# Performance work log

Measured on AMD Instinct MI355X. Metric: run time of the kernel, lower is better.

## Reference

```python
import jax, jax.numpy as jnp
import numpy as np
import math

HGT, WID = 24, 24          # shape2d
NUM_HEADS = 12
EMB = 768
HEAD_DIM = EMB // NUM_HEADS
N_GRID = HGT * WID         # 576 spatial tokens
N_TOK = N_GRID + 1         # +1 CLS token
BATCH = 32


def _rel_indices(h: int, w: int) -> np.ndarray:
    """[(h*w), (h*w)] indices into the (2h-1)*(2w-1) relative table."""
    y = np.arange(h)
    x = np.arange(w)
    y1, x1, y2, x2 = np.meshgrid(y, x, y, x, indexing='ij')
    idx = (y1 - y2 + h - 1) * (2 * w - 1) + (x1 - x2 + w - 1)
    return idx.reshape(h * w, h * w)


def setup_inputs() -> dict:
    key = jax.random.key(0)
    ks = jax.random.split(key, 6)
    s = 0.02
    return {
        "x": jax.random.normal(ks[0], (BATCH, N_TOK, EMB), dtype=jnp.float32),
        "Wq": jax.random.normal(ks[1], (EMB, EMB), dtype=jnp.float32) * s,
        "bq": jnp.zeros((EMB,), dtype=jnp.float32),
        "Wk": jax.random.normal(ks[2], (EMB, EMB), dtype=jnp.float32) * s,
        "bk": jnp.zeros((EMB,), dtype=jnp.float32),
        "Wv": jax.random.normal(ks[3], (EMB, EMB), dtype=jnp.float32) * s,
        "bv": jnp.zeros((EMB,), dtype=jnp.float32),
        "Wp": jax.random.normal(ks[4], (EMB, EMB), dtype=jnp.float32) * s,
        "bp": jnp.zeros((EMB,), dtype=jnp.float32),
        "rel_table": jax.random.normal(ks[5], ((2 * HGT - 1) * (2 * WID - 1), NUM_HEADS), dtype=jnp.float32) * s,
    }


def reference(x, Wq, bq, Wk, bk, Wv, bv, Wp, bp, rel_table):
    B, N, E = x.shape
    scale = 1.0 / math.sqrt(HEAD_DIM)

    def heads(t):  # [B,N,E] -> [B,H,N,hd]
        return t.reshape(B, N, NUM_HEADS, HEAD_DIM).transpose(0, 2, 1, 3)

    q = heads(x @ Wq.T + bq)
    k = heads(x @ Wk.T + bk)
    v = heads(x @ Wv.T + bv)

    scores = jnp.einsum('bhqd,bhkd->bhqk', q, k) * scale  # [B,H,N,N]

    # relative position bias on spatial tokens (skip CLS row/col)
    idx = jnp.asarray(_rel_indices(HGT, WID))              # [Ng,Ng]
    bias = rel_table[idx].transpose(2, 0, 1)               # [H,Ng,Ng]
    scores = scores.at[:, :, 1:, 1:].add(bias)

    attn = jax.nn.softmax(scores, axis=-1)
    out = jnp.einsum('bhqk,bhkd->bhqd', attn, v)           # [B,H,N,hd]
    out = out.transpose(0, 2, 1, 3).reshape(B, N, E)
    return out @ Wp.T + bp
```

## Files before the change

### kernel.cpp

```cpp
#include <hip/hip_runtime.h>
#include <stdint.h>

#define HGT   24
#define WID   24
#define NHEAD 12
#define EMB   768
#define HD    64
#define NGRID 576
#define NTOK  577
#define NPAD  640
#define BATCH 32
#define MROWS (BATCH * NTOK)
#define NKT   10
#define NQT   5
#define QKVC  (3 * EMB)

typedef __attribute__((ext_vector_type(8))) short bf16x8;
typedef __attribute__((ext_vector_type(4))) float f32x4;

__device__ __forceinline__ short f2bf(float f) {
    union { float f; unsigned u; } c; c.f = f;
    unsigned r = (c.u + 0x7FFFu + ((c.u >> 16) & 1u)) >> 16;
    return (short)(r & 0xFFFFu);
}
__device__ __forceinline__ float b2f(short s) {
    union { unsigned u; float f; } c; c.u = ((unsigned)(unsigned short)s) << 16;
    return c.f;
}

__device__ __forceinline__ void gload16(void* lds, const void* g) {
    __builtin_amdgcn_global_load_lds(
        (const __attribute__((address_space(1))) void*)g,
        (__attribute__((address_space(3))) void*)lds, 16, 0, 0);
}

__device__ __forceinline__ void wait_vm0_barrier() {
    asm volatile("s_waitcnt vmcnt(0)" ::: "memory");
    __builtin_amdgcn_s_barrier();
}

__device__ __forceinline__ int xcd_swizzle(int orig, int nwg) {
    int q = nwg >> 3, r = nwg & 7;
    int xcd = orig & 7, idx = orig >> 3;
    return (xcd < r) ? xcd * (q + 1) + idx : r * (q + 1) + (xcd - r) * q + idx;
}

__global__ void cast_f32_bf16(const float* __restrict__ src, short* __restrict__ dst, int n) {
    int i = (blockIdx.x * blockDim.x + threadIdx.x) * 4;
    int stride = gridDim.x * blockDim.x * 4;
    for (int j = i; j < n; j += stride) {
        float4 v = *(const float4*)(src + j);
        short4 o;
        o.x = f2bf(v.x); o.y = f2bf(v.y); o.z = f2bf(v.z); o.w = f2bf(v.w);
        *(short4*)(dst + j) = o;
    }
}

__global__ void bias_expand(const float* __restrict__ rel, short* __restrict__ be) {
    int q = blockIdx.x;
    int k = threadIdx.x;
    float v[NHEAD];
    if (k >= NTOK) {
#pragma unroll
        for (int h = 0; h < NHEAD; h++) v[h] = -1e30f;
    } else if (q == 0 || q >= NTOK || k == 0) {
#pragma unroll
        for (int h = 0; h < NHEAD; h++) v[h] = 0.f;
    } else {
        int i = q - 1, j = k - 1;
        int idx = ((i / WID) - (j / WID) + HGT - 1) * (2 * WID - 1)
                + ((i % WID) - (j % WID) + WID - 1);
        const float* rp = rel + (size_t)idx * NHEAD;
#pragma unroll
        for (int h = 0; h < NHEAD; h++) v[h] = rp[h];
    }
#pragma unroll
    for (int h = 0; h < NHEAD; h++)
        be[((size_t)h * NPAD + q) * NPAD + k] = f2bf(v[h]);
}

__global__ __launch_bounds__(256) void transpose_v(const short* __restrict__ qnat, short* __restrict__ vt) {
    __shared__ __align__(16) short T[64][72];
    int bi = blockIdx.x;
    int kt = bi % NKT;
    int h  = (bi / NKT) % NHEAD;
    int b  = bi / (NKT * NHEAD);
    int t  = threadIdx.x;

    int r  = t >> 2, cb = (t & 3) * 16;
    int key = kt * 64 + r; if (key >= NTOK) key = NTOK - 1;
    const short* src = qnat + (size_t)(b * NTOK + key) * QKVC + 2 * EMB + h * HD;
    *(int4*)&T[r][cb]     = *(const int4*)(src + cb);
    *(int4*)&T[r][cb + 8] = *(const int4*)(src + cb + 8);
    __syncthreads();

    int d = t >> 2, kb = (t & 3) * 16;
    short tmp[16];
#pragma unroll
    for (int s = 0; s < 16; s++) tmp[s] = T[kb + s][d];
    short* dst = vt + (((size_t)b * NHEAD + h) * HD + d) * NPAD + kt * 64 + kb;
    *(int4*)&dst[0] = *(int4*)&tmp[0];
    *(int4*)&dst[8] = *(int4*)&tmp[8];
}

template <int MODE>
__global__ __launch_bounds__(512) void gemm_bt(
    const short* __restrict__ A, const short* __restrict__ Bw,
    const float* __restrict__ b0, const float* __restrict__ b1, const float* __restrict__ b2,
    void* __restrict__ Outp, int M)
{
    constexpr int NC  = (MODE == 0) ? QKVC : EMB;
    constexpr int NBX = NC / 256;
    constexpr int K   = EMB;
    constexpr int NST = K / 32;

    __shared__ __align__(16) short Asl[4][256][32];
    __shared__ __align__(16) short Bsl[4][256][32];

    const int t    = threadIdx.x;
    const int lane = t & 63;
    const int w    = t >> 6;
    const int wm   = w >> 2;
    const int wn   = w & 3;
    const int lg   = lane >> 4;
    const int li   = lane & 15;

    const int nwg  = NBX * ((MROWS + 255) / 256);
    const int wgid = xcd_swizzle(blockIdx.x, nwg);
    const int tm   = (wgid / NBX) * 256;
    const int tn   = (wgid % NBX) * 256;

    const int drow = lane >> 2;
    const int lc   = (lane & 3) ^ ((lane >> 3) & 3);
    const int xsw  = (li >> 1) & 3;

    const short* agp[2];
    const short* bgp[2];
#pragma unroll
    for (int gi = 0; gi < 2; gi++) {
        int rm = tm + gi * 128 + w * 16 + drow; if (rm >= M) rm = M - 1;
        agp[gi] = A  + (size_t)rm * K + lc * 8;
        bgp[gi] = Bw + (size_t)(tn + gi * 128 + w * 16 + drow) * K + lc * 8;
    }

    f32x4 acc[8][4];
#pragma unroll
    for (int i = 0; i < 8; i++)
#pragma unroll
        for (int j = 0; j < 4; j++) acc[i][j] = (f32x4){0.f, 0.f, 0.f, 0.f};

#pragma unroll
    for (int ss = 0; ss < 3; ss++) {
        gload16(&Asl[ss][0 * 128 + w * 16][0], agp[0] + ss * 32);
        gload16(&Asl[ss][1 * 128 + w * 16][0], agp[1] + ss * 32);
        gload16(&Bsl[ss][0 * 128 + w * 16][0], bgp[0] + ss * 32);
        gload16(&Bsl[ss][1 * 128 + w * 16][0], bgp[1] + ss * 32);
    }

    for (int s = 0; s < NST; s++) {
        if (s < NST - 2)       asm volatile("s_waitcnt vmcnt(8)" ::: "memory");
        else if (s == NST - 2) asm volatile("s_waitcnt vmcnt(4)" ::: "memory");
        else                   asm volatile("s_waitcnt vmcnt(0)" ::: "memory");
        __builtin_amdgcn_s_barrier();

        const int cb = s & 3;
        bf16x8 af[8], bfv[4];
#pragma unroll
        for (int mi = 0; mi < 8; mi++)
            af[mi] = *(const bf16x8*)&Asl[cb][wm * 128 + mi * 16 + li][(lg ^ xsw) * 8];
#pragma unroll
        for (int nj = 0; nj < 4; nj++)
            bfv[nj] = *(const bf16x8*)&Bsl[cb][wn * 64 + nj * 16 + li][(lg ^ xsw) * 8];

        if (s + 3 < NST) {
            const int tb = (s + 3) & 3;
            const int ko = (s + 3) * 32;
            gload16(&Asl[tb][0 * 128 + w * 16][0], agp[0] + ko);
            gload16(&Asl[tb][1 * 128 + w * 16][0], agp[1] + ko);
            gload16(&Bsl[tb][0 * 128 + w * 16][0], bgp[0] + ko);
            gload16(&Bsl[tb][1 * 128 + w * 16][0], bgp[1] + ko);
        }

        __builtin_amdgcn_s_setprio(1);
#pragma unroll
        for (int mi = 0; mi < 8; mi++)
#pragma unroll
            for (int nj = 0; nj < 4; nj++)
                acc[mi][nj] = __builtin_amdgcn_mfma_f32_16x16x32_bf16(
                    bfv[nj], af[mi], acc[mi][nj], 0, 0, 0);
        __builtin_amdgcn_s_setprio(0);
    }

#pragma unroll
    for (int nj = 0; nj < 4; nj++) {
        const int ccb = tn + wn * 64 + nj * 16 + lg * 4;
        float4 bias4;
        if constexpr (MODE == 0) {
            int which = (ccb >= 2 * EMB) ? 2 : ((ccb >= EMB) ? 1 : 0);
            const float* bb = (which == 0) ? b0 : ((which == 1) ? b1 : b2);
            bias4 = *(const float4*)&bb[ccb - which * EMB];
        } else {
            bias4 = *(const float4*)&b0[ccb];
        }
#pragma unroll
        for (int mi = 0; mi < 8; mi++) {
            int m = tm + wm * 128 + mi * 16 + li;
            if (m >= M) continue;
            if constexpr (MODE == 0) {
                short4 o;
                o.x = f2bf(acc[mi][nj][0] + bias4.x);
                o.y = f2bf(acc[mi][nj][1] + bias4.y);
                o.z = f2bf(acc[mi][nj][2] + bias4.z);
                o.w = f2bf(acc[mi][nj][3] + bias4.w);
                *(short4*)&((short*)Outp)[(size_t)m * NC + ccb] = o;
            } else {
                float4 o;
                o.x = acc[mi][nj][0] + bias4.x;
                o.y = acc[mi][nj][1] + bias4.y;
                o.z = acc[mi][nj][2] + bias4.z;
                o.w = acc[mi][nj][3] + bias4.w;
                *(float4*)&((float*)Outp)[(size_t)m * NC + ccb] = o;
            }
        }
    }
}

__global__ __launch_bounds__(512) void attn_kernel(
    const short* __restrict__ qnat, const short* __restrict__ vt,
    const short* __restrict__ biasx, short* __restrict__ aout)
{
    __shared__ __align__(16) short Ksl[2][64][64];
    __shared__ __align__(16) short Vsl[2][64][64];
    __shared__ __align__(16) short Psl[8][16][72];

    const int wg = (blockIdx.x & 7) * (BATCH * NHEAD * NQT / 8) + (blockIdx.x >> 3);
    const int qt = wg % NQT;
    const int rest = wg / NQT;
    const int b  = rest & 31;
    const int h  = rest >> 5;

    const int t    = threadIdx.x;
    const int lane = t & 63;
    const int w    = t >> 6;
    const int lg   = lane >> 4;
    const int li   = lane & 15;
    const int xh   = li & 7;
    const int qbase = qt * 128;
    const int myq  = qbase + w * 16 + li;

    const short* qp  = qnat + (size_t)b * NTOK * QKVC + h * HD;
    const short* kp  = qp + EMB;
    const short* vtp = vt + ((size_t)b * NHEAD + h) * (size_t)HD * NPAD;
    const short* browq = biasx + ((size_t)h * NPAD + myq) * NPAD;

    bf16x8 qf[2];
    {
        int qrow = myq < NTOK ? myq : NTOK - 1;
        qf[0] = *(const bf16x8*)(qp + (size_t)qrow * QKVC + lg * 8);
        qf[1] = *(const bf16x8*)(qp + (size_t)qrow * QKVC + 32 + lg * 8);
    }

    float mrun = -1e30f, lrun = 0.f;
    f32x4 oacc[4];
#pragma unroll
    for (int d = 0; d < 4; d++) oacc[d] = (f32x4){0.f, 0.f, 0.f, 0.f};

    const int srow = w * 8 + (lane >> 3);
    const int cofs = ((lane & 7) ^ (lane >> 3)) * 8;

    {
        int key = srow; if (key >= NTOK) key = NTOK - 1;
        gload16(&Ksl[0][w * 8][0], kp + (size_t)key * QKVC + cofs);
        gload16(&Vsl[0][w * 8][0], vtp + (size_t)srow * NPAD + cofs);
    }
    wait_vm0_barrier();

    short (*Kc)[64] = Ksl[0], (*Kn)[64] = Ksl[1];
    short (*Vc)[64] = Vsl[0], (*Vn)[64] = Vsl[1];

    for (int kt = 0; kt < NKT; kt++) {
        if (kt + 1 < NKT) {
            int key = (kt + 1) * 64 + srow; if (key >= NTOK) key = NTOK - 1;
            gload16(&Kn[w * 8][0], kp + (size_t)key * QKVC + cofs);
            gload16(&Vn[w * 8][0], vtp + (size_t)srow * NPAD + (kt + 1) * 64 + cofs);
        }

        float pvv[4][4];
        __builtin_amdgcn_s_setprio(1);
#pragma unroll
        for (int j = 0; j < 4; j++) {
            short4 bs = *(const short4*)&browq[kt * 64 + j * 16 + lg * 4];
            bf16x8 ak0 = *(const bf16x8*)&Kc[j * 16 + li][(lg ^ xh) * 8];
            bf16x8 ak1 = *(const bf16x8*)&Kc[j * 16 + li][((4 + lg) ^ xh) * 8];
            f32x4 s = (f32x4){0.f, 0.f, 0.f, 0.f};
            s = __builtin_amdgcn_mfma_f32_16x16x32_bf16(ak0, qf[0], s, 0, 0, 0);
            s = __builtin_amdgcn_mfma_f32_16x16x32_bf16(ak1, qf[1], s, 0, 0, 0);
            pvv[j][0] = fmaf(s[0], 0.125f, b2f(bs.x));
            pvv[j][1] = fmaf(s[1], 0.125f, b2f(bs.y));
            pvv[j][2] = fmaf(s[2], 0.125f, b2f(bs.z));
            pvv[j][3] = fmaf(s[3], 0.125f, b2f(bs.w));
        }
        __builtin_amdgcn_s_setprio(0);

        float mt = pvv[0][0];
#pragma unroll
        for (int j = 0; j < 4; j++)
#pragma unroll
            for (int r = 0; r < 4; r++) mt = fmaxf(mt, pvv[j][r]);
        mt = fmaxf(mt, __shfl_xor(mt, 16, 64));
        mt = fmaxf(mt, __shfl_xor(mt, 32, 64));
        float nm  = fmaxf(mrun, mt);
        float fac = __expf(mrun - nm);
        float rs  = 0.f;
#pragma unroll
        for (int j = 0; j < 4; j++)
#pragma unroll
            for (int r = 0; r < 4; r++) {
                float p = __expf(pvv[j][r] - nm);
                pvv[j][r] = p;
                rs += p;
            }
        rs += __shfl_xor(rs, 16, 64);
        rs += __shfl_xor(rs, 32, 64);
        lrun = lrun * fac + rs;
        mrun = nm;
#pragma unroll
        for (int d = 0; d < 4; d++) oacc[d] *= fac;

#pragma unroll
        for (int j = 0; j < 4; j++) {
            short4 ps;
            ps.x = f2bf(pvv[j][0]); ps.y = f2bf(pvv[j][1]);
            ps.z = f2bf(pvv[j][2]); ps.w = f2bf(pvv[j][3]);
            *(short4*)&Psl[w][li][j * 16 + lg * 4] = ps;
        }

        __builtin_amdgcn_s_setprio(1);
#pragma unroll
        for (int dd = 0; dd < 4; dd++) {
#pragma unroll
            for (int kk = 0; kk < 2; kk++) {
                bf16x8 av = *(const bf16x8*)&Vc[dd * 16 + li][((kk * 4 + lg) ^ xh) * 8];
                bf16x8 pb = *(const bf16x8*)&Psl[w][li][kk * 32 + lg * 8];
                oacc[dd] = __builtin_amdgcn_mfma_f32_16x16x32_bf16(av, pb, oacc[dd], 0, 0, 0);
            }
        }
        __builtin_amdgcn_s_setprio(0);

        wait_vm0_barrier();
        short (*tp)[64];
        tp = Kc; Kc = Kn; Kn = tp;
        tp = Vc; Vc = Vn; Vn = tp;
    }

    if (myq < NTOK) {
        float inv = 1.0f / lrun;
        short* op = aout + ((size_t)b * NTOK + myq) * EMB + h * HD;
#pragma unroll
        for (int dd = 0; dd < 4; dd++) {
            short4 o;
            o.x = f2bf(oacc[dd][0] * inv);
            o.y = f2bf(oacc[dd][1] * inv);
            o.z = f2bf(oacc[dd][2] * inv);
            o.w = f2bf(oacc[dd][3] * inv);
            *(short4*)&op[dd * 16 + lg * 4] = o;
        }
    }
}

extern "C" void kernel_launch(void* const* d_in, const int* in_sizes, int n_in,
                              void* d_out, int out_size, void* d_ws, size_t ws_size,
                              hipStream_t stream) {
    (void)in_sizes; (void)n_in; (void)out_size; (void)ws_size;
    const float* x   = (const float*)d_in[0];
    const float* Wq  = (const float*)d_in[1];
    const float* bq  = (const float*)d_in[2];
    const float* Wk  = (const float*)d_in[3];
    const float* bk  = (const float*)d_in[4];
    const float* Wv  = (const float*)d_in[5];
    const float* bv  = (const float*)d_in[6];
    const float* Wp  = (const float*)d_in[7];
    const float* bp  = (const float*)d_in[8];
    const float* rel = (const float*)d_in[9];

    const size_t WN = (size_t)EMB * EMB;
    short* Wb   = (short*)d_ws;
    short* Wpb  = Wb + 3 * WN;
    short* qnat = Wpb + WN;
    short* xb   = qnat + (size_t)MROWS * QKVC;
    short* aout = xb;
    short* vtb  = xb + (size_t)MROWS * EMB;
    short* bexp = vtb + (size_t)BATCH * NHEAD * HD * NPAD;

    const int XN = MROWS * EMB;
    const int MT = (MROWS + 255) / 256;
    cast_f32_bf16<<<576, 256, 0, stream>>>(Wq, Wb, (int)WN);
    cast_f32_bf16<<<576, 256, 0, stream>>>(Wk, Wb + WN, (int)WN);
    cast_f32_bf16<<<576, 256, 0, stream>>>(Wv, Wb + 2 * WN, (int)WN);
    cast_f32_bf16<<<576, 256, 0, stream>>>(Wp, Wpb, (int)WN);
    cast_f32_bf16<<<13848, 256, 0, stream>>>(x, xb, XN);
    bias_expand<<<NPAD, NPAD, 0, stream>>>(rel, bexp);

    gemm_bt<0><<<9 * MT, 512, 0, stream>>>(xb, Wb, bq, bk, bv, qnat, MROWS);
    transpose_v<<<BATCH * NHEAD * NKT, 256, 0, stream>>>(qnat, vtb);
    attn_kernel<<<BATCH * NHEAD * NQT, 512, 0, stream>>>(qnat, vtb, bexp, aout);
    gemm_bt<1><<<3 * MT, 512, 0, stream>>>(aout, Wpb, bp, bp, bp, d_out, MROWS);
}
```

Before: 282.5 us.

## Use exp2 softmax with lazy rescaling, packed bf16 converts, swizzled P tile, bias prefetch

Folds log2(e) into the score scale and the precomputed bias table so the softmax can use a native exp2, and skips the running-max rescale of the accumulators unless the new max exceeds the old one by more than a threshold. The bias row for the next key tile is now prefetched into registers one iteration early. The P staging tile loses its padding and uses an XOR swizzle instead, and float-to-bf16 conversions are packed two at a time through the HIP bf16 intrinsic across the cast, GEMM epilogue and attention kernels. The lazy rescale lets unnormalized values grow by up to 2^8 before correction, which adds some numerical risk.

```diff
diff --git a/kernel.cpp b/kernel.cpp
--- a/kernel.cpp
+++ b/kernel.cpp
@@ -1,4 +1,5 @@
 #include <hip/hip_runtime.h>
+#include <hip/hip_bf16.h>
 #include <stdint.h>
 
 #define HGT   24
@@ -27,6 +28,18 @@
     union { unsigned u; float f; } c; c.u = ((unsigned)(unsigned short)s) << 16;
     return c.f;
 }
+__device__ __forceinline__ unsigned pk2bf(float a, float b) {
+    __hip_bfloat162 h = __float22bfloat162_rn(make_float2(a, b));
+    union { __hip_bfloat162 h; unsigned u; } c; c.h = h;
+    return c.u;
+}
+__device__ __forceinline__ float fexp2(float x) {
+#if __has_builtin(__builtin_amdgcn_exp2f)
+    return __builtin_amdgcn_exp2f(x);
+#else
+    return __expf(x * 0.69314718f);
+#endif
+}
 
 __device__ __forceinline__ void gload16(void* lds, const void* g) {
     __builtin_amdgcn_global_load_lds(
@@ -50,13 +63,15 @@
     int stride = gridDim.x * blockDim.x * 4;
     for (int j = i; j < n; j += stride) {
         float4 v = *(const float4*)(src + j);
-        short4 o;
-        o.x = f2bf(v.x); o.y = f2bf(v.y); o.z = f2bf(v.z); o.w = f2bf(v.w);
-        *(short4*)(dst + j) = o;
+        uint2 o;
+        o.x = pk2bf(v.x, v.y);
+        o.y = pk2bf(v.z, v.w);
+        *(uint2*)(dst + j) = o;
     }
 }
 
 __global__ void bias_expand(const float* __restrict__ rel, short* __restrict__ be) {
+    const float L2E = 1.44269504f;
     int q = blockIdx.x;
     int k = threadIdx.x;
     float v[NHEAD];
@@ -76,7 +91,7 @@
     }
 #pragma unroll
     for (int h = 0; h < NHEAD; h++)
-        be[((size_t)h * NPAD + q) * NPAD + k] = f2bf(v[h]);
+        be[((size_t)h * NPAD + q) * NPAD + k] = f2bf(v[h] * L2E);
 }
 
 __global__ __launch_bounds__(256) void transpose_v(const short* __restrict__ qnat, short* __restrict__ vt) {
@@ -207,12 +222,10 @@
             int m = tm + wm * 128 + mi * 16 + li;
             if (m >= M) continue;
             if constexpr (MODE == 0) {
-                short4 o;
-                o.x = f2bf(acc[mi][nj][0] + bias4.x);
-                o.y = f2bf(acc[mi][nj][1] + bias4.y);
-                o.z = f2bf(acc[mi][nj][2] + bias4.z);
-                o.w = f2bf(acc[mi][nj][3] + bias4.w);
-                *(short4*)&((short*)Outp)[(size_t)m * NC + ccb] = o;
+                uint2 o;
+                o.x = pk2bf(acc[mi][nj][0] + bias4.x, acc[mi][nj][1] + bias4.y);
+                o.y = pk2bf(acc[mi][nj][2] + bias4.z, acc[mi][nj][3] + bias4.w);
+                *(uint2*)&((short*)Outp)[(size_t)m * NC + ccb] = o;
             } else {
                 float4 o;
                 o.x = acc[mi][nj][0] + bias4.x;
@@ -231,7 +244,7 @@
 {
     __shared__ __align__(16) short Ksl[2][64][64];
     __shared__ __align__(16) short Vsl[2][64][64];
-    __shared__ __align__(16) short Psl[8][16][72];
+    __shared__ __align__(16) short Psl[8][16][64];
 
     const int wg = (blockIdx.x & 7) * (BATCH * NHEAD * NQT / 8) + (blockIdx.x >> 3);
     const int qt = wg % NQT;
@@ -248,6 +261,8 @@
     const int qbase = qt * 128;
     const int myq  = qbase + w * 16 + li;
 
+    const float SCL = 0.18033688f;
+
     const short* qp  = qnat + (size_t)b * NTOK * QKVC + h * HD;
     const short* kp  = qp + EMB;
     const short* vtp = vt + ((size_t)b * NHEAD + h) * (size_t)HD * NPAD;
@@ -273,6 +288,9 @@
         gload16(&Ksl[0][w * 8][0], kp + (size_t)key * QKVC + cofs);
         gload16(&Vsl[0][w * 8][0], vtp + (size_t)srow * NPAD + cofs);
     }
+    short4 bcur[4];
+#pragma unroll
+    for (int j = 0; j < 4; j++) bcur[j] = *(const short4*)&browq[j * 16 + lg * 4];
     wait_vm0_barrier();
 
     short (*Kc)[64] = Ksl[0], (*Kn)[64] = Ksl[1];
@@ -284,21 +302,27 @@
             gload16(&Kn[w * 8][0], kp + (size_t)key * QKVC + cofs);
             gload16(&Vn[w * 8][0], vtp + (size_t)srow * NPAD + (kt + 1) * 64 + cofs);
         }
+        short4 bnxt[4];
+        {
+            int ktn = (kt + 1 < NKT) ? kt + 1 : kt;
+#pragma unroll
+            for (int j = 0; j < 4; j++)
+                bnxt[j] = *(const short4*)&browq[ktn * 64 + j * 16 + lg * 4];
+        }
 
         float pvv[4][4];
         __builtin_amdgcn_s_setprio(1);
 #pragma unroll
         for (int j = 0; j < 4; j++) {
-            short4 bs = *(const short4*)&browq[kt * 64 + j * 16 + lg * 4];
             bf16x8 ak0 = *(const bf16x8*)&Kc[j * 16 + li][(lg ^ xh) * 8];
             bf16x8 ak1 = *(const bf16x8*)&Kc[j * 16 + li][((4 + lg) ^ xh) * 8];
             f32x4 s = (f32x4){0.f, 0.f, 0.f, 0.f};
             s = __builtin_amdgcn_mfma_f32_16x16x32_bf16(ak0, qf[0], s, 0, 0, 0);
             s = __builtin_amdgcn_mfma_f32_16x16x32_bf16(ak1, qf[1], s, 0, 0, 0);
-            pvv[j][0] = fmaf(s[0], 0.125f, b2f(bs.x));
-            pvv[j][1] = fmaf(s[1], 0.125f, b2f(bs.y));
-            pvv[j][2] = fmaf(s[2], 0.125f, b2f(bs.z));
-            pvv[j][3] = fmaf(s[3], 0.125f, b2f(bs.w));
+            pvv[j][0] = fmaf(s[0], SCL, b2f(bcur[j].x));
+            pvv[j][1] = fmaf(s[1], SCL, b2f(bcur[j].y));
+            pvv[j][2] = fmaf(s[2], SCL, b2f(bcur[j].z));
+            pvv[j][3] = fmaf(s[3], SCL, b2f(bcur[j].w));
         }
         __builtin_amdgcn_s_setprio(0);
 
@@ -309,30 +333,33 @@
             for (int r = 0; r < 4; r++) mt = fmaxf(mt, pvv[j][r]);
         mt = fmaxf(mt, __shfl_xor(mt, 16, 64));
         mt = fmaxf(mt, __shfl_xor(mt, 32, 64));
-        float nm  = fmaxf(mrun, mt);
-        float fac = __expf(mrun - nm);
-        float rs  = 0.f;
+        if (__any(mt > mrun + 8.0f)) {
+            float nm  = fmaxf(mrun, mt);
+            float fac = fexp2(mrun - nm);
+            mrun = nm;
+            lrun *= fac;
+#pragma unroll
+            for (int d = 0; d < 4; d++) oacc[d] *= fac;
+        }
+        float rs = 0.f;
 #pragma unroll
         for (int j = 0; j < 4; j++)
 #pragma unroll
             for (int r = 0; r < 4; r++) {
-                float p = __expf(pvv[j][r] - nm);
+                float p = fexp2(pvv[j][r] - mrun);
                 pvv[j][r] = p;
                 rs += p;
             }
         rs += __shfl_xor(rs, 16, 64);
         rs += __shfl_xor(rs, 32, 64);
-        lrun = lrun * fac + rs;
-        mrun = nm;
-#pragma unroll
-        for (int d = 0; d < 4; d++) oacc[d] *= fac;
+        lrun += rs;
 
 #pragma unroll
         for (int j = 0; j < 4; j++) {
-            short4 ps;
-            ps.x = f2bf(pvv[j][0]); ps.y = f2bf(pvv[j][1]);
-            ps.z = f2bf(pvv[j][2]); ps.w = f2bf(pvv[j][3]);
-            *(short4*)&Psl[w][li][j * 16 + lg * 4] = ps;
+            uint2 pw;
+            pw.x = pk2bf(pvv[j][0], pvv[j][1]);
+            pw.y = pk2bf(pvv[j][2], pvv[j][3]);
+            *(uint2*)&Psl[w][li][(((2 * j + (lg >> 1)) ^ xh) * 8) + (lg & 1) * 4] = pw;
         }
 
         __builtin_amdgcn_s_setprio(1);
@@ -341,7 +368,7 @@
 #pragma unroll
             for (int kk = 0; kk < 2; kk++) {
                 bf16x8 av = *(const bf16x8*)&Vc[dd * 16 + li][((kk * 4 + lg) ^ xh) * 8];
-                bf16x8 pb = *(const bf16x8*)&Psl[w][li][kk * 32 + lg * 8];
+                bf16x8 pb = *(const bf16x8*)&Psl[w][li][((kk * 4 + lg) ^ xh) * 8];
                 oacc[dd] = __builtin_amdgcn_mfma_f32_16x16x32_bf16(av, pb, oacc[dd], 0, 0, 0);
             }
         }
@@ -351,6 +378,8 @@
         short (*tp)[64];
         tp = Kc; Kc = Kn; Kn = tp;
         tp = Vc; Vc = Vn; Vn = tp;
+#pragma unroll
+        for (int j = 0; j < 4; j++) bcur[j] = bnxt[j];
     }
 
     if (myq < NTOK) {
@@ -358,12 +387,10 @@
         short* op = aout + ((size_t)b * NTOK + myq) * EMB + h * HD;
 #pragma unroll
         for (int dd = 0; dd < 4; dd++) {
-            short4 o;
-            o.x = f2bf(oacc[dd][0] * inv);
-            o.y = f2bf(oacc[dd][1] * inv);
-            o.z = f2bf(oacc[dd][2] * inv);
-            o.w = f2bf(oacc[dd][3] * inv);
-            *(short4*)&op[dd * 16 + lg * 4] = o;
+            uint2 o;
+            o.x = pk2bf(oacc[dd][0] * inv, oacc[dd][1] * inv);
+            o.y = pk2bf(oacc[dd][2] * inv, oacc[dd][3] * inv);
+            *(uint2*)&op[dd * 16 + lg * 4] = o;
         }
     }
 }
```

Result: no change. 282.8 us (+0.1%).
